# Kernel tuning notes

Measured on AMD Instinct MI355X. Metric: run time of the kernel, lower is better.

The kernel has to match this reference:

```python
import jax, jax.numpy as jnp
import numpy as np

B, N, F_IN, F_OUT = 8, 2048, 256, 256
H, D = 8, 32
LN_EPS = 1e-5


def setup_inputs() -> dict:
    key = jax.random.key(0)
    ks = jax.random.split(key, 8)
    s = 1.0 / np.sqrt(F_IN)
    so = 1.0 / np.sqrt(H * D)
    return {
        "x": jax.random.normal(ks[0], (B, N, F_IN), dtype=jnp.float32),
        "adj": jax.random.randint(ks[1], (B, N, N), 0, 2, dtype=jnp.int32),
        "Wq": jax.random.uniform(ks[2], (F_IN, H * D), jnp.float32, -s, s),
        "bq": jnp.zeros((H * D,), jnp.float32),
        "Wk": jax.random.uniform(ks[3], (F_IN, H * D), jnp.float32, -s, s),
        "bk": jnp.zeros((H * D,), jnp.float32),
        "Wv": jax.random.uniform(ks[4], (F_IN, H * D), jnp.float32, -s, s),
        "bv": jnp.zeros((H * D,), jnp.float32),
        "Wo": jax.random.uniform(ks[5], (H * D, F_OUT), jnp.float32, -so, so),
        "bo": jnp.zeros((F_OUT,), jnp.float32),
        "gamma": jnp.ones((F_OUT,), jnp.float32),
        "beta": jnp.zeros((F_OUT,), jnp.float32),
    }


def reference(x, adj, Wq, bq, Wk, bk, Wv, bv, Wo, bo, gamma, beta):
    b, n, _ = x.shape
    # QKV projections -> [B, H, N, D]
    q = (x @ Wq + bq).reshape(b, n, H, D).transpose(0, 2, 1, 3)
    k = (x @ Wk + bk).reshape(b, n, H, D).transpose(0, 2, 1, 3)
    v = (x @ Wv + bv).reshape(b, n, H, D).transpose(0, 2, 1, 3)
    # masked attention scores [B, H, N, N]
    scores = jnp.einsum('bhqd,bhkd->bhqk', q, k) / np.sqrt(D).astype(np.float32)
    scores = jnp.where(adj[:, None, :, :] == 0, -jnp.inf, scores)
    attn = jax.nn.softmax(scores, axis=-1)
    # dropout layers are identity in eval mode
    out = jnp.einsum('bhqk,bhkd->bhqd', attn, v)
    out = out.transpose(0, 2, 1, 3).reshape(b, n, H * D)
    out = out @ Wo + bo
    # LayerNorm
    mu = out.mean(-1, keepdims=True)
    var = out.var(-1, keepdims=True)
    out = (out - mu) * jax.lax.rsqrt(var + LN_EPS) * gamma + beta
    return out, attn.mean(axis=1)
```

## Files before the change

kernel.cpp:

```cpp
#include <hip/hip_runtime.h>


typedef __attribute__((ext_vector_type(8))) short short8;
typedef __attribute__((ext_vector_type(4))) float f32x4;
typedef __attribute__((ext_vector_type(4))) unsigned short us4;
typedef unsigned short u16;
typedef unsigned int u32;

#define SC2 0.25503486127240555f

__device__ __forceinline__ u16 cvt(float f) {
  __bf16 h = (__bf16)f;
  union { __bf16 h; u16 u; } v; v.h = h; return v.u;
}

__global__ __launch_bounds__(256) void k_prep(
    const int* __restrict__ adj, u32* __restrict__ packed,
    const float* __restrict__ w0, const float* __restrict__ w1,
    const float* __restrict__ w2, const float* __restrict__ w3,
    u16* __restrict__ o0, u16* __restrict__ o1,
    u16* __restrict__ o2, u16* __restrict__ o3) {
  int bid = blockIdx.x;
  if (bid < 256) {
    int z = bid >> 6, rem = bid & 63;
    const float* in; u16* out;
    if (z == 0) { in = w0; out = o0; }
    else if (z == 1) { in = w1; out = o1; }
    else if (z == 2) { in = w2; out = o2; }
    else { in = w3; out = o3; }
    __shared__ u16 t[32][33];
    int tx = threadIdx.x & 31, ty = threadIdx.x >> 5;
    int x0 = (rem & 7) * 32, y0 = (rem >> 3) * 32;
    for (int j = 0; j < 32; j += 8)
      t[ty + j][tx] = cvt(in[(y0 + ty + j) * 256 + x0 + tx]);
    __syncthreads();
    for (int j = 0; j < 32; j += 8)
      out[(x0 + ty + j) * 256 + y0 + tx] = t[tx][ty + j];
  } else {
    int lane = threadIdx.x & 63;
#pragma unroll 4
    for (int it = 0; it < 64; it++) {
      unsigned int i = ((bid - 256) * 64u + it) * 256u + threadIdx.x;
      unsigned long long m = __ballot(adj[i] != 0);
      if (lane == 0)       packed[i >> 5] = (u32)m;
      else if (lane == 32) packed[i >> 5] = (u32)(m >> 32);
    }
  }
}

__global__ __launch_bounds__(256) void k_qkv(
    const float* __restrict__ x, const u16* __restrict__ wt,
    const float* __restrict__ bq, const float* __restrict__ bk,
    const float* __restrict__ bv,
    u16* __restrict__ qw, u16* __restrict__ kw, u16* __restrict__ vt) {
  int l = threadIdx.x & 63, w = threadIdx.x >> 6;
  int lr = l & 15, lg = l >> 4;
  int row0 = blockIdx.y * 64 + w * 16;
  int c0 = blockIdx.x * 64;
  f32x4 acc[4] = {};
  const float* xr = x + (size_t)(row0 + lr) * 256 + lg * 8;
  const u16* wr = wt + (c0 + lr) * 256 + lg * 8;
  for (int k0 = 0; k0 < 256; k0 += 32) {
    f32x4 f0 = *(const f32x4*)(xr + k0);
    f32x4 f1 = *(const f32x4*)(xr + k0 + 4);
    short8 a;
    a[0] = (short)cvt(f0[0]); a[1] = (short)cvt(f0[1]);
    a[2] = (short)cvt(f0[2]); a[3] = (short)cvt(f0[3]);
    a[4] = (short)cvt(f1[0]); a[5] = (short)cvt(f1[1]);
    a[6] = (short)cvt(f1[2]); a[7] = (short)cvt(f1[3]);
#pragma unroll
    for (int ct = 0; ct < 4; ct++) {
      short8 bb = *(const short8*)(wr + ct * 16 * 256 + k0);
      acc[ct] = __builtin_amdgcn_mfma_f32_16x16x32_bf16(a, bb, acc[ct], 0, 0, 0);
    }
  }
  int mtx = blockIdx.x >> 2;
  const float* bias = (mtx == 0) ? bq : ((mtx == 1) ? bk : bv);
  int b = row0 >> 11, nbase = row0 & 2047;
#pragma unroll
  for (int ct = 0; ct < 4; ct++) {
    int cc = (c0 + ct * 16 + lr) & 255;
    int h = cc >> 5, d = cc & 31;
    float bs = bias[cc];
    if (mtx < 2) {
      u16* dst = (mtx == 0) ? qw : kw;
      float sc = (mtx == 0) ? SC2 : 1.0f;
#pragma unroll
      for (int rr = 0; rr < 4; rr++) {
        int n = nbase + lg * 4 + rr;
        dst[((b * 8 + h) * 2048 + n) * 32 + d] = cvt((acc[ct][rr] + bs) * sc);
      }
    } else {
      us4 pk;
#pragma unroll
      for (int rr = 0; rr < 4; rr++) pk[rr] = cvt(acc[ct][rr] + bs);
      *(us4*)(vt + (size_t)((b * 8 + h) * 32 + d) * 2048 + nbase + lg * 4) = pk;
    }
  }
}

__global__ __launch_bounds__(512) void k_attn(
    const u16* __restrict__ qw, const u16* __restrict__ kw,
    const u16* __restrict__ vt, const u32* __restrict__ packed,
    u16* __restrict__ ao, float* __restrict__ out2) {
  __shared__ __align__(16) u16 P[8][2048];
  __shared__ float lsbuf[8][32];
  int l = threadIdx.x & 63, wv = threadIdx.x >> 6;
  int lr = l & 15, lg = l >> 4;
  int b = blockIdx.x & 7, q0 = (blockIdx.x >> 3) * 32;
  const u32* pkb = packed + (size_t)(b * 2048 + q0) * 64;

  {
    int h = wv;
    const u16* qb = qw + (size_t)((b * 8 + h) * 2048 + q0) * 32;
    const u16* kb = kw + (size_t)((b * 8 + h) * 2048) * 32;
    const u16* vb = vt + (size_t)((b * 8 + h) * 32) * 2048;
    short8 qf0 = *(const short8*)(qb + lr * 32 + lg * 8);
    short8 qf1 = *(const short8*)(qb + (16 + lr) * 32 + lg * 8);
    u16* Pt = &P[h][0];
    float ls0 = 0.f, ls1 = 0.f;
    f32x4 acc[2][2] = {};
#pragma unroll 2
    for (int ch = 0; ch < 32; ch++) {
      uint2 m0 = *(const uint2*)(pkb + lr * 64 + ch * 2);
      uint2 m1 = *(const uint2*)(pkb + (16 + lr) * 64 + ch * 2);
#pragma unroll
      for (int j = 0; j < 4; j++) {
        short8 kf = *(const short8*)(kb + (size_t)(ch * 64 + j * 16 + lr) * 32 + lg * 8);
        f32x4 z = {};
        f32x4 s0 = __builtin_amdgcn_mfma_f32_16x16x32_bf16(kf, qf0, z, 0, 0, 0);
        f32x4 s1 = __builtin_amdgcn_mfma_f32_16x16x32_bf16(kf, qf1, z, 0, 0, 0);
        u32 w0 = ((j & 2) ? m0.y : m0.x) >> ((j & 1) * 16 + lg * 4);
        u32 w1 = ((j & 2) ? m1.y : m1.x) >> ((j & 1) * 16 + lg * 4);
        us4 p0, p1;
#pragma unroll
        for (int rr = 0; rr < 4; rr++) {
          float e0 = __builtin_exp2f(s0[rr]);
          float e1 = __builtin_exp2f(s1[rr]);
          float em0 = ((w0 >> rr) & 1u) ? e0 : 0.0f;
          float em1 = ((w1 >> rr) & 1u) ? e1 : 0.0f;
          ls0 += em0; ls1 += em1;
          p0[rr] = cvt(em0); p1[rr] = cvt(em1);
        }
        int slot = 2 * j + (lg >> 1), offs = (lg & 1) * 4;
        *(us4*)(Pt + lr * 64 + ((slot ^ (lr & 7)) << 3) + offs) = p0;
        *(us4*)(Pt + (16 + lr) * 64 + ((slot ^ (lr & 7)) << 3) + offs) = p1;
      }
#pragma unroll
      for (int k2 = 0; k2 < 2; k2++) {
        short8 pa0 = *(const short8*)(Pt + lr * 64 +
                        (((k2 * 4 + lg) ^ (lr & 7)) << 3));
        short8 pa1 = *(const short8*)(Pt + (16 + lr) * 64 +
                        (((k2 * 4 + lg) ^ (lr & 7)) << 3));
#pragma unroll
        for (int dt = 0; dt < 2; dt++) {
          short8 vf = *(const short8*)(vb + (size_t)(dt * 16 + lr) * 2048 +
                                       ch * 64 + k2 * 32 + lg * 8);
          acc[0][dt] = __builtin_amdgcn_mfma_f32_16x16x32_bf16(pa0, vf, acc[0][dt], 0, 0, 0);
          acc[1][dt] = __builtin_amdgcn_mfma_f32_16x16x32_bf16(pa1, vf, acc[1][dt], 0, 0, 0);
        }
      }
    }
    ls0 += __shfl_xor(ls0, 16); ls0 += __shfl_xor(ls0, 32);
    ls1 += __shfl_xor(ls1, 16); ls1 += __shfl_xor(ls1, 32);
    ls0 = fmaxf(ls0, 1e-30f); ls1 = fmaxf(ls1, 1e-30f);
    if (l < 16) { lsbuf[h][lr] = ls0; lsbuf[h][16 + lr] = ls1; }
    float r0 = 1.0f / ls0, r1 = 1.0f / ls1;
#pragma unroll
    for (int qs = 0; qs < 2; qs++)
#pragma unroll
      for (int rr = 0; rr < 4; rr++) {
        float rq = __shfl(qs == 0 ? r0 : r1, lg * 4 + rr);
#pragma unroll
        for (int dt = 0; dt < 2; dt++) {
          int n = q0 + qs * 16 + lg * 4 + rr;
          ao[(size_t)(b * 2048 + n) * 256 + h * 32 + dt * 16 + lr] =
              cvt(acc[qs][dt][rr] * rq);
        }
      }
  }
  __syncthreads();

  {
    int qh = (wv >> 2) * 16;
    int c0 = (wv & 3) * 8;
    short8 qfh[8];
    float rls8[8];
#pragma unroll
    for (int hh = 0; hh < 8; hh++) {
      qfh[hh] = *(const short8*)(qw +
          (size_t)((b * 8 + hh) * 2048 + q0 + qh + lr) * 32 + lg * 8);
      rls8[hh] = 0.125f / lsbuf[hh][qh + lr];
    }
    const u32* pkb2 = packed + (size_t)(b * 2048 + q0 + qh) * 64;
#pragma unroll 2
    for (int ch = c0; ch < c0 + 8; ch++) {
      uint2 mw = *(const uint2*)(pkb2 + lr * 64 + ch * 2);
#pragma unroll
      for (int j = 0; j < 4; j++) {
        f32x4 macc = {};
#pragma unroll
        for (int hh = 0; hh < 8; hh++) {
          const u16* kbh = kw + (size_t)((b * 8 + hh) * 2048) * 32;
          short8 kf = *(const short8*)(kbh +
              (size_t)(ch * 64 + j * 16 + lr) * 32 + lg * 8);
          f32x4 z = {};
          f32x4 s = __builtin_amdgcn_mfma_f32_16x16x32_bf16(kf, qfh[hh], z, 0, 0, 0);
#pragma unroll
          for (int rr = 0; rr < 4; rr++)
            macc[rr] = fmaf(__builtin_exp2f(s[rr]), rls8[hh], macc[rr]);
        }
        u32 wj = ((j & 2) ? mw.y : mw.x) >> ((j & 1) * 16 + lg * 4);
        f32x4 o;
#pragma unroll
        for (int rr = 0; rr < 4; rr++)
          o[rr] = ((wj >> rr) & 1u) ? macc[rr] : 0.0f;
        *(f32x4*)(out2 + (size_t)(b * 2048 + q0 + qh + lr) * 2048 +
                  ch * 64 + j * 16 + lg * 4) = o;
      }
    }
  }
}

__global__ __launch_bounds__(256) void k_oproj(
    const u16* __restrict__ ao, const u16* __restrict__ wto,
    const float* __restrict__ bo, const float* __restrict__ gamma,
    const float* __restrict__ beta, float* __restrict__ out) {
  int l = threadIdx.x & 63, w = threadIdx.x >> 6;
  int lr = l & 15, lg = l >> 4;
  int row0 = blockIdx.x * 64 + w * 16;
  f32x4 acc[16] = {};
  const u16* ar = ao + (size_t)(row0 + lr) * 256 + lg * 8;
  const u16* wr = wto + lr * 256 + lg * 8;
  for (int k0 = 0; k0 < 256; k0 += 32) {
    short8 a = *(const short8*)(ar + k0);
#pragma unroll
    for (int ct = 0; ct < 16; ct++) {
      short8 bb = *(const short8*)(wr + ct * 16 * 256 + k0);
      acc[ct] = __builtin_amdgcn_mfma_f32_16x16x32_bf16(a, bb, acc[ct], 0, 0, 0);
    }
  }
  float sum[4] = {0, 0, 0, 0}, sq[4] = {0, 0, 0, 0};
#pragma unroll
  for (int ct = 0; ct < 16; ct++) {
    float bs = bo[ct * 16 + lr];
#pragma unroll
    for (int rr = 0; rr < 4; rr++) {
      float v = acc[ct][rr] + bs;
      acc[ct][rr] = v;
      sum[rr] += v; sq[rr] += v * v;
    }
  }
#pragma unroll
  for (int rr = 0; rr < 4; rr++) {
    float s = sum[rr], q = sq[rr];
    s += __shfl_xor(s, 1); s += __shfl_xor(s, 2);
    s += __shfl_xor(s, 4); s += __shfl_xor(s, 8);
    q += __shfl_xor(q, 1); q += __shfl_xor(q, 2);
    q += __shfl_xor(q, 4); q += __shfl_xor(q, 8);
    float mu = s * (1.0f / 256.0f);
    float var = fmaxf(q * (1.0f / 256.0f) - mu * mu, 0.0f);
    sum[rr] = mu;
    sq[rr] = rsqrtf(var + 1e-5f);
  }
#pragma unroll
  for (int ct = 0; ct < 16; ct++) {
    float g = gamma[ct * 16 + lr], be = beta[ct * 16 + lr];
#pragma unroll
    for (int rr = 0; rr < 4; rr++) {
      int n = row0 + lg * 4 + rr;
      out[(size_t)n * 256 + ct * 16 + lr] =
          ((acc[ct][rr] - sum[rr]) * sq[rr]) * g + be;
    }
  }
}

extern "C" void kernel_launch(void* const* d_in, const int* in_sizes, int n_in,
                              void* d_out, int out_size, void* d_ws, size_t ws_size,
                              hipStream_t stream) {
  const float* x    = (const float*)d_in[0];
  const int*   adj  = (const int*)d_in[1];
  const float* Wq   = (const float*)d_in[2];
  const float* bq   = (const float*)d_in[3];
  const float* Wk   = (const float*)d_in[4];
  const float* bk   = (const float*)d_in[5];
  const float* Wv   = (const float*)d_in[6];
  const float* bv   = (const float*)d_in[7];
  const float* Wo   = (const float*)d_in[8];
  const float* bo   = (const float*)d_in[9];
  const float* gamma= (const float*)d_in[10];
  const float* beta = (const float*)d_in[11];

  char* ws = (char*)d_ws;
  u16* wtq = (u16*)(ws + 0);
  u16* wtk = (u16*)(ws + 131072);
  u16* wtv = (u16*)(ws + 262144);
  u16* wto = (u16*)(ws + 393216);
  u16* qw  = (u16*)(ws + 524288);
  u16* kw  = (u16*)(ws + 8912896);
  u16* vt  = (u16*)(ws + 17301504);
  u16* ao  = (u16*)(ws + 25690112);
  u32* pk  = (u32*)(ws + 34078720);

  float* out  = (float*)d_out;
  float* out2 = out + (size_t)8 * 2048 * 256;

  k_prep<<<dim3(2304), dim3(256), 0, stream>>>(adj, pk, Wq, Wk, Wv, Wo,
                                               wtq, wtk, wtv, wto);
  k_qkv<<<dim3(12, 256), dim3(256), 0, stream>>>(x, wtq, bq, bk, bv, qw, kw, vt);
  k_attn<<<dim3(512), dim3(512), 0, stream>>>(qw, kw, vt, pk, ao, out2);
  k_oproj<<<dim3(256), dim3(256), 0, stream>>>(ao, wto, bo, gamma, beta, out);
}
```

Before: 365.3 us.

## Fuse output projection and LayerNorm into attention; merge adj packing with QKV

The output projection and LayerNorm now run at the end of the attention kernel. The attention output is kept in shared memory as bf16 instead of being written to global memory and reloaded by a separate kernel, and LayerNorm statistics are reduced across waves through a small LDS buffer. The adjacency bit-packing blocks move out of the weight-transpose kernel into the QKV projection launch, so packing overlaps with the GEMM and one launch is removed. The cost is extra LDS per attention block, which may lower occupancy, and each block re-reads the output-projection weights.

```diff
diff --git a/kernel.cpp b/kernel.cpp
--- a/kernel.cpp
+++ b/kernel.cpp
@@ -15,48 +15,50 @@
 }
 
 __global__ __launch_bounds__(256) void k_prep(
-    const int* __restrict__ adj, u32* __restrict__ packed,
     const float* __restrict__ w0, const float* __restrict__ w1,
     const float* __restrict__ w2, const float* __restrict__ w3,
     u16* __restrict__ o0, u16* __restrict__ o1,
     u16* __restrict__ o2, u16* __restrict__ o3) {
   int bid = blockIdx.x;
-  if (bid < 256) {
-    int z = bid >> 6, rem = bid & 63;
-    const float* in; u16* out;
-    if (z == 0) { in = w0; out = o0; }
-    else if (z == 1) { in = w1; out = o1; }
-    else if (z == 2) { in = w2; out = o2; }
-    else { in = w3; out = o3; }
-    __shared__ u16 t[32][33];
-    int tx = threadIdx.x & 31, ty = threadIdx.x >> 5;
-    int x0 = (rem & 7) * 32, y0 = (rem >> 3) * 32;
-    for (int j = 0; j < 32; j += 8)
-      t[ty + j][tx] = cvt(in[(y0 + ty + j) * 256 + x0 + tx]);
-    __syncthreads();
-    for (int j = 0; j < 32; j += 8)
-      out[(x0 + ty + j) * 256 + y0 + tx] = t[tx][ty + j];
-  } else {
+  int z = bid >> 6, rem = bid & 63;
+  const float* in; u16* out;
+  if (z == 0) { in = w0; out = o0; }
+  else if (z == 1) { in = w1; out = o1; }
+  else if (z == 2) { in = w2; out = o2; }
+  else { in = w3; out = o3; }
+  __shared__ u16 t[32][33];
+  int tx = threadIdx.x & 31, ty = threadIdx.x >> 5;
+  int x0 = (rem & 7) * 32, y0 = (rem >> 3) * 32;
+  for (int j = 0; j < 32; j += 8)
+    t[ty + j][tx] = cvt(in[(y0 + ty + j) * 256 + x0 + tx]);
+  __syncthreads();
+  for (int j = 0; j < 32; j += 8)
+    out[(x0 + ty + j) * 256 + y0 + tx] = t[tx][ty + j];
+}
+
+__global__ __launch_bounds__(256) void k_qkvpack(
+    const float* __restrict__ x, const u16* __restrict__ wt,
+    const float* __restrict__ bq, const float* __restrict__ bk,
+    const float* __restrict__ bv,
+    u16* __restrict__ qw, u16* __restrict__ kw, u16* __restrict__ vt,
+    const int* __restrict__ adj, u32* __restrict__ packed) {
+  int bid = blockIdx.x;
+  if (bid >= 3072) {
     int lane = threadIdx.x & 63;
 #pragma unroll 4
     for (int it = 0; it < 64; it++) {
-      unsigned int i = ((bid - 256) * 64u + it) * 256u + threadIdx.x;
+      unsigned int i = ((bid - 3072) * 64u + it) * 256u + threadIdx.x;
       unsigned long long m = __ballot(adj[i] != 0);
       if (lane == 0)       packed[i >> 5] = (u32)m;
       else if (lane == 32) packed[i >> 5] = (u32)(m >> 32);
     }
-  }
-}
-
-__global__ __launch_bounds__(256) void k_qkv(
-    const float* __restrict__ x, const u16* __restrict__ wt,
-    const float* __restrict__ bq, const float* __restrict__ bk,
-    const float* __restrict__ bv,
-    u16* __restrict__ qw, u16* __restrict__ kw, u16* __restrict__ vt) {
+    return;
+  }
+  int bx = bid % 12, by = bid / 12;
   int l = threadIdx.x & 63, w = threadIdx.x >> 6;
   int lr = l & 15, lg = l >> 4;
-  int row0 = blockIdx.y * 64 + w * 16;
-  int c0 = blockIdx.x * 64;
+  int row0 = by * 64 + w * 16;
+  int c0 = bx * 64;
   f32x4 acc[4] = {};
   const float* xr = x + (size_t)(row0 + lr) * 256 + lg * 8;
   const u16* wr = wt + (c0 + lr) * 256 + lg * 8;
@@ -74,7 +76,7 @@
       acc[ct] = __builtin_amdgcn_mfma_f32_16x16x32_bf16(a, bb, acc[ct], 0, 0, 0);
     }
   }
-  int mtx = blockIdx.x >> 2;
+  int mtx = bx >> 2;
   const float* bias = (mtx == 0) ? bq : ((mtx == 1) ? bk : bv);
   int b = row0 >> 11, nbase = row0 & 2047;
 #pragma unroll
@@ -102,9 +104,13 @@
 __global__ __launch_bounds__(512) void k_attn(
     const u16* __restrict__ qw, const u16* __restrict__ kw,
     const u16* __restrict__ vt, const u32* __restrict__ packed,
-    u16* __restrict__ ao, float* __restrict__ out2) {
+    const u16* __restrict__ wto, const float* __restrict__ bo,
+    const float* __restrict__ gamma, const float* __restrict__ beta,
+    float* __restrict__ out, float* __restrict__ out2) {
   __shared__ __align__(16) u16 P[8][2048];
+  __shared__ __align__(16) u16 aoL[32 * 264];
   __shared__ float lsbuf[8][32];
+  __shared__ float lnb[32][4][2];
   int l = threadIdx.x & 63, wv = threadIdx.x >> 6;
   int lr = l & 15, lg = l >> 4;
   int b = blockIdx.x & 7, q0 = (blockIdx.x >> 3) * 32;
@@ -173,8 +179,7 @@
         float rq = __shfl(qs == 0 ? r0 : r1, lg * 4 + rr);
 #pragma unroll
         for (int dt = 0; dt < 2; dt++) {
-          int n = q0 + qs * 16 + lg * 4 + rr;
-          ao[(size_t)(b * 2048 + n) * 256 + h * 32 + dt * 16 + lr] =
+          aoL[(qs * 16 + lg * 4 + rr) * 264 + h * 32 + dt * 16 + lr] =
               cvt(acc[qs][dt][rr] * rq);
         }
       }
@@ -220,57 +225,63 @@
       }
     }
   }
-}
-
-__global__ __launch_bounds__(256) void k_oproj(
-    const u16* __restrict__ ao, const u16* __restrict__ wto,
-    const float* __restrict__ bo, const float* __restrict__ gamma,
-    const float* __restrict__ beta, float* __restrict__ out) {
-  int l = threadIdx.x & 63, w = threadIdx.x >> 6;
-  int lr = l & 15, lg = l >> 4;
-  int row0 = blockIdx.x * 64 + w * 16;
-  f32x4 acc[16] = {};
-  const u16* ar = ao + (size_t)(row0 + lr) * 256 + lg * 8;
-  const u16* wr = wto + lr * 256 + lg * 8;
-  for (int k0 = 0; k0 < 256; k0 += 32) {
-    short8 a = *(const short8*)(ar + k0);
-#pragma unroll
-    for (int ct = 0; ct < 16; ct++) {
-      short8 bb = *(const short8*)(wr + ct * 16 * 256 + k0);
-      acc[ct] = __builtin_amdgcn_mfma_f32_16x16x32_bf16(a, bb, acc[ct], 0, 0, 0);
-    }
-  }
-  float sum[4] = {0, 0, 0, 0}, sq[4] = {0, 0, 0, 0};
-#pragma unroll
-  for (int ct = 0; ct < 16; ct++) {
-    float bs = bo[ct * 16 + lr];
+
+  {
+    int rh = wv & 1, cg = wv >> 1;
+    f32x4 acc[4] = {};
+    const u16* wr = wto + (cg * 64 + lr) * 256 + lg * 8;
+    for (int k0 = 0; k0 < 256; k0 += 32) {
+      short8 a = *(const short8*)(&aoL[(rh * 16 + lr) * 264 + k0 + lg * 8]);
+#pragma unroll
+      for (int ct = 0; ct < 4; ct++) {
+        short8 bb = *(const short8*)(wr + ct * 16 * 256 + k0);
+        acc[ct] = __builtin_amdgcn_mfma_f32_16x16x32_bf16(a, bb, acc[ct], 0, 0, 0);
+      }
+    }
+    float sum[4] = {0, 0, 0, 0}, sq[4] = {0, 0, 0, 0};
+#pragma unroll
+    for (int ct = 0; ct < 4; ct++) {
+      float bs = bo[cg * 64 + ct * 16 + lr];
+#pragma unroll
+      for (int rr = 0; rr < 4; rr++) {
+        float v = acc[ct][rr] + bs;
+        acc[ct][rr] = v;
+        sum[rr] += v; sq[rr] += v * v;
+      }
+    }
 #pragma unroll
     for (int rr = 0; rr < 4; rr++) {
-      float v = acc[ct][rr] + bs;
-      acc[ct][rr] = v;
-      sum[rr] += v; sq[rr] += v * v;
-    }
-  }
-#pragma unroll
-  for (int rr = 0; rr < 4; rr++) {
-    float s = sum[rr], q = sq[rr];
-    s += __shfl_xor(s, 1); s += __shfl_xor(s, 2);
-    s += __shfl_xor(s, 4); s += __shfl_xor(s, 8);
-    q += __shfl_xor(q, 1); q += __shfl_xor(q, 2);
-    q += __shfl_xor(q, 4); q += __shfl_xor(q, 8);
-    float mu = s * (1.0f / 256.0f);
-    float var = fmaxf(q * (1.0f / 256.0f) - mu * mu, 0.0f);
-    sum[rr] = mu;
-    sq[rr] = rsqrtf(var + 1e-5f);
-  }
-#pragma unroll
-  for (int ct = 0; ct < 16; ct++) {
-    float g = gamma[ct * 16 + lr], be = beta[ct * 16 + lr];
+      float s = sum[rr], q = sq[rr];
+      s += __shfl_xor(s, 1); s += __shfl_xor(s, 2);
+      s += __shfl_xor(s, 4); s += __shfl_xor(s, 8);
+      q += __shfl_xor(q, 1); q += __shfl_xor(q, 2);
+      q += __shfl_xor(q, 4); q += __shfl_xor(q, 8);
+      sum[rr] = s; sq[rr] = q;
+    }
+    if ((l & 15) == 0) {
+#pragma unroll
+      for (int rr = 0; rr < 4; rr++) {
+        int row = rh * 16 + lg * 4 + rr;
+        lnb[row][cg][0] = sum[rr];
+        lnb[row][cg][1] = sq[rr];
+      }
+    }
+    __syncthreads();
 #pragma unroll
     for (int rr = 0; rr < 4; rr++) {
-      int n = row0 + lg * 4 + rr;
-      out[(size_t)n * 256 + ct * 16 + lr] =
-          ((acc[ct][rr] - sum[rr]) * sq[rr]) * g + be;
+      int row = rh * 16 + lg * 4 + rr;
+      float S = lnb[row][0][0] + lnb[row][1][0] + lnb[row][2][0] + lnb[row][3][0];
+      float Q = lnb[row][0][1] + lnb[row][1][1] + lnb[row][2][1] + lnb[row][3][1];
+      float mu = S * (1.0f / 256.0f);
+      float var = fmaxf(Q * (1.0f / 256.0f) - mu * mu, 0.0f);
+      float rs = rsqrtf(var + 1e-5f);
+      size_t obase = (size_t)(b * 2048 + q0 + row) * 256 + cg * 64;
+#pragma unroll
+      for (int ct = 0; ct < 4; ct++) {
+        float g = gamma[cg * 64 + ct * 16 + lr];
+        float be = beta[cg * 64 + ct * 16 + lr];
+        out[obase + ct * 16 + lr] = (acc[ct][rr] - mu) * rs * g + be;
+      }
     }
   }
 }
@@ -299,15 +310,15 @@
   u16* qw  = (u16*)(ws + 524288);
   u16* kw  = (u16*)(ws + 8912896);
   u16* vt  = (u16*)(ws + 17301504);
-  u16* ao  = (u16*)(ws + 25690112);
   u32* pk  = (u32*)(ws + 34078720);
 
   float* out  = (float*)d_out;
   float* out2 = out + (size_t)8 * 2048 * 256;
 
-  k_prep<<<dim3(2304), dim3(256), 0, stream>>>(adj, pk, Wq, Wk, Wv, Wo,
-                                               wtq, wtk, wtv, wto);
-  k_qkv<<<dim3(12, 256), dim3(256), 0, stream>>>(x, wtq, bq, bk, bv, qw, kw, vt);
-  k_attn<<<dim3(512), dim3(512), 0, stream>>>(qw, kw, vt, pk, ao, out2);
-  k_oproj<<<dim3(256), dim3(256), 0, stream>>>(ao, wto, bo, gamma, beta, out);
-}
+  k_prep<<<dim3(256), dim3(256), 0, stream>>>(Wq, Wk, Wv, Wo,
+                                              wtq, wtk, wtv, wto);
+  k_qkvpack<<<dim3(5120), dim3(256), 0, stream>>>(x, wtq, bq, bk, bv,
+                                                  qw, kw, vt, adj, pk);
+  k_attn<<<dim3(512), dim3(512), 0, stream>>>(qw, kw, vt, pk, wto, bo,
+                                              gamma, beta, out, out2);
+}
```

After: 382.6 us. +4.7%, slower.
